# Performance work log

Measured on AMD Instinct MI355X. Metric: run time of the kernel, lower is better.

Reference implementation:

```python
import jax, jax.numpy as jnp
import numpy as np

H = 1024   # hidden_size
NH = 16    # num heads
HD = H // NH


def setup_inputs() -> dict:
    key = jax.random.key(0)
    ks = jax.random.split(key, 6)
    B, S = 4, 2048
    hidden_states = jax.random.normal(ks[0], (B, S, H), dtype=jnp.float32)
    attention_mask = jnp.zeros((B, S), dtype=jnp.float32)  # additive mask
    scale = 1.0 / np.sqrt(H)
    Wq = jax.random.normal(ks[1], (H, H), dtype=jnp.float32) * scale
    Wk = jax.random.normal(ks[2], (H, H), dtype=jnp.float32) * scale
    Wv = jax.random.normal(ks[3], (H, H), dtype=jnp.float32) * scale
    Wo = jax.random.normal(ks[4], (H, H), dtype=jnp.float32) * scale
    return {"hidden_states": hidden_states, "attention_mask": attention_mask,
            "Wq": Wq, "Wk": Wk, "Wv": Wv, "Wo": Wo}


def reference(hidden_states, attention_mask, Wq, Wk, Wv, Wo):
    B, S, _ = hidden_states.shape
    scaling = HD ** -0.5
    # nn.Linear: y = x @ W.T ; split heads -> [B, NH, S, HD]
    def heads(x, W):
        return (x @ W.T).reshape(B, S, NH, HD).transpose(0, 2, 1, 3)
    q = heads(hidden_states, Wq)
    k = heads(hidden_states, Wk)
    v = heads(hidden_states, Wv)
    scores = jnp.einsum('bhqd,bhkd->bhqk', q, k) * scaling
    scores = scores + attention_mask[:, None, None, :]
    weights = jax.nn.softmax(scores, axis=-1)
    attn = jnp.einsum('bhqk,bhkd->bhqd', weights, v)
    attn = attn.transpose(0, 2, 1, 3).reshape(B, S, H)
    return attn @ Wo.T
```

## Files before the change

### kernel.cpp

```cpp
#include <hip/hip_runtime.h>
#include <hip/hip_bf16.h>

#define B_ 4
#define S_ 2048
#define H_ 1024
#define NH_ 16
#define HD_ 64
#define QSCALE 0.1803368801111204f

typedef __bf16 bf16_t;
typedef bf16_t bf16x8 __attribute__((ext_vector_type(8)));
typedef bf16_t bf16x4 __attribute__((ext_vector_type(4)));
typedef float f32x4 __attribute__((ext_vector_type(4)));

__device__ __forceinline__ f32x4 mfma16(bf16x8 a, bf16x8 b, f32x4 c) {
  return __builtin_amdgcn_mfma_f32_16x16x32_bf16(a, b, c, 0, 0, 0);
}

__device__ __forceinline__ void gll16(const bf16_t* g, bf16_t* l) {
  __builtin_amdgcn_global_load_lds(
      (const __attribute__((address_space(1))) void*)g,
      (__attribute__((address_space(3))) void*)l, 16, 0, 0);
}

__device__ __forceinline__ bf16x8 frag64(const bf16_t* lds, int row,
                                         int kchunk) {
  return *(const bf16x8*)((const char*)lds + row * 128 +
                          ((kchunk ^ (row & 7)) << 4));
}

__device__ __forceinline__ void stage128(const bf16_t* gbase, int gstride,
                                         bf16_t* lds, int w, int lane) {
#pragma unroll
  for (int j = 0; j < 4; ++j) {
    int seg = w * 4 + j;
    int row = seg * 8 + (lane >> 3);
    int chunk = (lane & 7) ^ (row & 7);
    gll16(gbase + (size_t)row * gstride + chunk * 8, lds + seg * 512);
  }
}

__global__ __launch_bounds__(256) void cvt_all(
    const float* __restrict__ X, const float* __restrict__ Wq,
    const float* __restrict__ Wk, const float* __restrict__ Wv,
    const float* __restrict__ Wo,
    bf16_t* __restrict__ Xb, bf16_t* __restrict__ Wqb,
    bf16_t* __restrict__ Wkb, bf16_t* __restrict__ Wvb,
    bf16_t* __restrict__ Wob) {
  size_t i = ((size_t)blockIdx.x * 256 + threadIdx.x) * 4;
  const float* src;
  bf16_t* dst;
  size_t off;
  float scale = 1.0f;
  if (i < 8388608) {
    src = X; dst = Xb; off = i;
  } else {
    size_t j = i - 8388608;
    int w = (int)(j >> 20);
    off = j & 1048575;
    switch (w) {
      case 0: src = Wq; dst = Wqb; scale = QSCALE; break;
      case 1: src = Wk; dst = Wkb; break;
      case 2: src = Wv; dst = Wvb; break;
      default: src = Wo; dst = Wob; break;
    }
  }
  float4 v = *(const float4*)(src + off);
  bf16x4 o = {(bf16_t)(v.x * scale), (bf16_t)(v.y * scale),
              (bf16_t)(v.z * scale), (bf16_t)(v.w * scale)};
  *(bf16x4*)(dst + off) = o;
}

__device__ __forceinline__ void gemm_core(const bf16_t* __restrict__ A,
                                          const bf16_t* __restrict__ Bw,
                                          int Mb, int Nb, bf16_t* As,
                                          bf16_t* Bs, f32x4 (*acc)[4], int w,
                                          int lane, int quad, int l15, int wm,
                                          int wn) {
  for (int kb = 0; kb < 16; ++kb) {
    stage128(A + (size_t)Mb * 1024 + kb * 64, 1024, As, w, lane);
    stage128(Bw + (size_t)Nb * 1024 + kb * 64, 1024, Bs, w, lane);
    __syncthreads();
#pragma unroll
    for (int kt = 0; kt < 2; ++kt) {
      bf16x8 af[4], bfr[4];
#pragma unroll
      for (int i = 0; i < 4; ++i) {
        af[i] = frag64(As, wm * 64 + i * 16 + l15, kt * 4 + quad);
        bfr[i] = frag64(Bs, wn * 64 + i * 16 + l15, kt * 4 + quad);
      }
#pragma unroll
      for (int mt = 0; mt < 4; ++mt)
#pragma unroll
        for (int nt = 0; nt < 4; ++nt)
          acc[mt][nt] = mfma16(af[mt], bfr[nt], acc[mt][nt]);
    }
    __syncthreads();
  }
}

__global__ __launch_bounds__(256) void gemm_qkv(
    const bf16_t* __restrict__ Xb, const bf16_t* __restrict__ Wqb,
    const bf16_t* __restrict__ Wkb, const bf16_t* __restrict__ Wvb,
    bf16_t* __restrict__ q_ws, bf16_t* __restrict__ k_ws,
    bf16_t* __restrict__ vt_ws) {
  __shared__ __align__(16) bf16_t As[8192];
  __shared__ __align__(16) bf16_t Bs[8192];
  int w = threadIdx.x >> 6, lane = threadIdx.x & 63;
  int quad = lane >> 4, l15 = lane & 15;
  int wm = w >> 1, wn = w & 1;
  int z = blockIdx.z;
  const bf16_t* A = (z == 2) ? Wvb : Xb;
  const bf16_t* Bw = (z == 0) ? Wqb : ((z == 1) ? Wkb : Xb);
  int Mb = (z == 2) ? blockIdx.y * 128 : blockIdx.x * 128;
  int Nb = (z == 2) ? blockIdx.x * 128 : blockIdx.y * 128;
  f32x4 acc[4][4] = {};
  gemm_core(A, Bw, Mb, Nb, As, Bs, acc, w, lane, quad, l15, wm, wn);
  if (z != 2) {
    bf16_t* O = (z == 0) ? q_ws : k_ws;
#pragma unroll
    for (int mt = 0; mt < 4; ++mt) {
      int m0t = Mb + wm * 64 + mt * 16;
#pragma unroll
      for (int nt = 0; nt < 4; ++nt) {
        int n0t = Nb + wn * 64 + nt * 16;
        int h = n0t >> 6, d = (n0t & 63) + l15;
#pragma unroll
        for (int r = 0; r < 4; ++r) {
          int tok = m0t + quad * 4 + r;
          int b = tok >> 11, s = tok & 2047;
          O[(((size_t)b * NH_ + h) * S_ + s) * HD_ + d] = (bf16_t)acc[mt][nt][r];
        }
      }
    }
  } else {
#pragma unroll
    for (int mt = 0; mt < 4; ++mt) {
      int m0t = Mb + wm * 64 + mt * 16;
#pragma unroll
      for (int nt = 0; nt < 4; ++nt) {
        int n0t = Nb + wn * 64 + nt * 16;
#pragma unroll
        for (int r = 0; r < 4; ++r) {
          int dg = m0t + quad * 4 + r;
          int hh = dg >> 6, d = dg & 63;
          int tok = n0t + l15;
          int b = tok >> 11, s = tok & 2047;
          vt_ws[((size_t)(b * NH_ + hh) * HD_ + d) * S_ + s] =
              (bf16_t)acc[mt][nt][r];
        }
      }
    }
  }
}

__global__ __launch_bounds__(256) void gemm_out(
    const bf16_t* __restrict__ A, const bf16_t* __restrict__ Bw,
    float* __restrict__ out) {
  __shared__ __align__(16) bf16_t As[8192];
  __shared__ __align__(16) bf16_t Bs[8192];
  int w = threadIdx.x >> 6, lane = threadIdx.x & 63;
  int quad = lane >> 4, l15 = lane & 15;
  int wm = w >> 1, wn = w & 1;
  int Mb = blockIdx.x * 128, Nb = blockIdx.y * 128;
  f32x4 acc[4][4] = {};
  gemm_core(A, Bw, Mb, Nb, As, Bs, acc, w, lane, quad, l15, wm, wn);
#pragma unroll
  for (int mt = 0; mt < 4; ++mt) {
    int m0t = Mb + wm * 64 + mt * 16;
#pragma unroll
    for (int nt = 0; nt < 4; ++nt) {
      int n0t = Nb + wn * 64 + nt * 16;
#pragma unroll
      for (int r = 0; r < 4; ++r)
        out[(size_t)(m0t + quad * 4 + r) * 1024 + n0t + l15] = acc[mt][nt][r];
    }
  }
}

__global__ __launch_bounds__(256, 4) void attn_fused(
    const bf16_t* __restrict__ Q, const bf16_t* __restrict__ K,
    const bf16_t* __restrict__ Vt, const float* __restrict__ mask,
    bf16_t* __restrict__ Oa) {
  __shared__ __align__(16) bf16_t Ks[4096];
  __shared__ __align__(16) bf16_t Vs[4096];
  __shared__ __align__(16) bf16_t Ps[4][32 * 72];
  int w = threadIdx.x >> 6, lane = threadIdx.x & 63;
  int quad = lane >> 4, l15 = lane & 15;
  int bh = blockIdx.y;
  int b = bh >> 4, h = bh & 15;
  int q0 = blockIdx.x * 128 + w * 32;
  const bf16_t* Qh = Q + (size_t)bh * (S_ * HD_);
  const bf16_t* Kh = K + (size_t)bh * (S_ * HD_);
  const bf16_t* Vh = Vt + (size_t)bh * (HD_ * S_);
  const float* mb = mask + b * S_;
  bf16_t* pw = Ps[w];
  const float LOG2E = 1.4426950408889634f;
  const bf16_t one_b = (bf16_t)1.0f;
  bf16x8 ones = {one_b, one_b, one_b, one_b, one_b, one_b, one_b, one_b};

  int srow[2], schunk[2], soff[2];
#pragma unroll
  for (int j = 0; j < 2; ++j) {
    int seg = w * 2 + j;
    srow[j] = seg * 8 + (lane >> 3);
    schunk[j] = (lane & 7) ^ (srow[j] & 7);
    soff[j] = seg * 512 + lane * 8;
  }

  bf16x8 qf[2][2];
#pragma unroll
  for (int nt = 0; nt < 2; ++nt)
#pragma unroll
    for (int kt = 0; kt < 2; ++kt)
      qf[nt][kt] = *(const bf16x8*)(Qh + (size_t)(q0 + nt * 16 + l15) * HD_ +
                                    kt * 32 + quad * 8);

  f32x4 oc[4][2] = {};
  f32x4 lc[2] = {};

  bf16x8 kreg[2], vreg[2];
#pragma unroll
  for (int j = 0; j < 2; ++j) {
    kreg[j] = *(const bf16x8*)(Kh + (size_t)srow[j] * HD_ + schunk[j] * 8);
    vreg[j] = *(const bf16x8*)(Vh + (size_t)srow[j] * S_ + schunk[j] * 8);
  }

  for (int c = 0; c < 32; ++c) {
    __syncthreads();
#pragma unroll
    for (int j = 0; j < 2; ++j) {
      *(bf16x8*)(Ks + soff[j]) = kreg[j];
      *(bf16x8*)(Vs + soff[j]) = vreg[j];
    }
    __syncthreads();
    if (c + 1 < 32) {
      const bf16_t* Kc = Kh + (size_t)(c + 1) * 64 * HD_;
      const bf16_t* Vc = Vh + (size_t)(c + 1) * 64;
#pragma unroll
      for (int j = 0; j < 2; ++j) {
        kreg[j] = *(const bf16x8*)(Kc + (size_t)srow[j] * HD_ + schunk[j] * 8);
        vreg[j] = *(const bf16x8*)(Vc + (size_t)srow[j] * S_ + schunk[j] * 8);
      }
    }
    f32x4 sc[4][2] = {};
#pragma unroll
    for (int kt = 0; kt < 2; ++kt) {
      bf16x8 kf[4];
#pragma unroll
      for (int mt = 0; mt < 4; ++mt)
        kf[mt] = frag64(Ks, mt * 16 + l15, kt * 4 + quad);
#pragma unroll
      for (int mt = 0; mt < 4; ++mt)
#pragma unroll
        for (int nt = 0; nt < 2; ++nt)
          sc[mt][nt] = mfma16(kf[mt], qf[nt][kt], sc[mt][nt]);
    }
#pragma unroll
    for (int mt = 0; mt < 4; ++mt) {
      f32x4 mk = *(const f32x4*)(mb + c * 64 + mt * 16 + quad * 4);
      f32x4 mlv = mk * LOG2E;
#pragma unroll
      for (int nt = 0; nt < 2; ++nt) {
        f32x4 e = sc[mt][nt] + mlv;
        f32x4 p;
#pragma unroll
        for (int r = 0; r < 4; ++r) p[r] = __builtin_exp2f(e[r]);
        bf16x4 p4 = {(bf16_t)p[0], (bf16_t)p[1], (bf16_t)p[2], (bf16_t)p[3]};
        *(bf16x4*)(pw + (nt * 16 + l15) * 72 + mt * 16 + quad * 4) = p4;
      }
    }
#pragma unroll
    for (int kt = 0; kt < 2; ++kt) {
      bf16x8 pf[2];
#pragma unroll
      for (int nt = 0; nt < 2; ++nt)
        pf[nt] = *(const bf16x8*)(pw + (nt * 16 + l15) * 72 + kt * 32 +
                                  quad * 8);
      lc[0] = mfma16(ones, pf[0], lc[0]);
      lc[1] = mfma16(ones, pf[1], lc[1]);
#pragma unroll
      for (int dt = 0; dt < 4; ++dt) {
        bf16x8 vf = frag64(Vs, dt * 16 + l15, kt * 4 + quad);
#pragma unroll
        for (int nt = 0; nt < 2; ++nt)
          oc[dt][nt] = mfma16(vf, pf[nt], oc[dt][nt]);
      }
    }
  }
  float inv[2] = {1.0f / lc[0][0], 1.0f / lc[1][0]};
#pragma unroll
  for (int dt = 0; dt < 4; ++dt)
#pragma unroll
    for (int nt = 0; nt < 2; ++nt) {
      bf16x4 o4;
#pragma unroll
      for (int r = 0; r < 4; ++r) o4[r] = (bf16_t)(oc[dt][nt][r] * inv[nt]);
      size_t tok = (size_t)b * S_ + q0 + nt * 16 + l15;
      *(bf16x4*)(Oa + tok * H_ + h * HD_ + dt * 16 + quad * 4) = o4;
    }
}

extern "C" void kernel_launch(void* const* d_in, const int* in_sizes, int n_in,
                              void* d_out, int out_size, void* d_ws,
                              size_t ws_size, hipStream_t stream) {
  const float* hs   = (const float*)d_in[0];
  const float* mask = (const float*)d_in[1];
  const float* Wq   = (const float*)d_in[2];
  const float* Wk   = (const float*)d_in[3];
  const float* Wv   = (const float*)d_in[4];
  const float* Wo   = (const float*)d_in[5];
  float* out = (float*)d_out;

  char* p = (char*)d_ws;
  bf16_t* Xb  = (bf16_t*)p; p += (size_t)8192 * 1024 * 2;
  bf16_t* Wqb = (bf16_t*)p; p += (size_t)1024 * 1024 * 2;
  bf16_t* Wkb = (bf16_t*)p; p += (size_t)1024 * 1024 * 2;
  bf16_t* Wvb = (bf16_t*)p; p += (size_t)1024 * 1024 * 2;
  bf16_t* Wob = (bf16_t*)p; p += (size_t)1024 * 1024 * 2;
  bf16_t* q_ws  = (bf16_t*)p; p += (size_t)8192 * 1024 * 2;
  bf16_t* k_ws  = (bf16_t*)p; p += (size_t)8192 * 1024 * 2;
  bf16_t* vt_ws = (bf16_t*)p; p += (size_t)8192 * 1024 * 2;
  bf16_t* attn_b = Xb;

  cvt_all<<<12288, 256, 0, stream>>>(hs, Wq, Wk, Wv, Wo, Xb, Wqb, Wkb, Wvb,
                                     Wob);
  gemm_qkv<<<dim3(64, 8, 3), 256, 0, stream>>>(Xb, Wqb, Wkb, Wvb, q_ws, k_ws,
                                               vt_ws);
  attn_fused<<<dim3(16, 64), 256, 0, stream>>>(q_ws, k_ws, vt_ws, mask,
                                               attn_b);
  gemm_out<<<dim3(64, 8), 256, 0, stream>>>(attn_b, Wob, out);
}
```

Baseline: 298.9 us.

## Double-buffer K/V shared tiles and prefetch mask in attention kernel

Uses two LDS buffers for K and V so the next chunk is stored into the alternate buffer while the current one is consumed. This cuts the per-iteration barriers from two to one and prefetches global loads two chunks ahead. The mask values are also loaded one chunk early into registers. The cost is more LDS and registers, so launch bounds drop from 4 to 3 blocks per CU, which lowers occupancy.

Measured after the change: 292.2 us. 1.02x faster.

```diff
diff --git a/kernel.cpp b/kernel.cpp
--- a/kernel.cpp
+++ b/kernel.cpp
@@ -178,12 +178,12 @@
   }
 }
 
-__global__ __launch_bounds__(256, 4) void attn_fused(
+__global__ __launch_bounds__(256, 3) void attn_fused(
     const bf16_t* __restrict__ Q, const bf16_t* __restrict__ K,
     const bf16_t* __restrict__ Vt, const float* __restrict__ mask,
     bf16_t* __restrict__ Oa) {
-  __shared__ __align__(16) bf16_t Ks[4096];
-  __shared__ __align__(16) bf16_t Vs[4096];
+  __shared__ __align__(16) bf16_t Ks[2][4096];
+  __shared__ __align__(16) bf16_t Vs[2][4096];
   __shared__ __align__(16) bf16_t Ps[4][32 * 72];
   int w = threadIdx.x >> 6, lane = threadIdx.x & 63;
   int quad = lane >> 4, l15 = lane & 15;
@@ -225,31 +225,56 @@
     kreg[j] = *(const bf16x8*)(Kh + (size_t)srow[j] * HD_ + schunk[j] * 8);
     vreg[j] = *(const bf16x8*)(Vh + (size_t)srow[j] * S_ + schunk[j] * 8);
   }
+#pragma unroll
+  for (int j = 0; j < 2; ++j) {
+    *(bf16x8*)(&Ks[0][0] + soff[j]) = kreg[j];
+    *(bf16x8*)(&Vs[0][0] + soff[j]) = vreg[j];
+  }
+#pragma unroll
+  for (int j = 0; j < 2; ++j) {
+    kreg[j] = *(const bf16x8*)(Kh + (size_t)(64 * HD_) +
+                               (size_t)srow[j] * HD_ + schunk[j] * 8);
+    vreg[j] = *(const bf16x8*)(Vh + 64 + (size_t)srow[j] * S_ + schunk[j] * 8);
+  }
+  f32x4 mreg[4];
+#pragma unroll
+  for (int mt = 0; mt < 4; ++mt)
+    mreg[mt] = *(const f32x4*)(mb + mt * 16 + quad * 4);
+  __syncthreads();
 
   for (int c = 0; c < 32; ++c) {
-    __syncthreads();
-#pragma unroll
-    for (int j = 0; j < 2; ++j) {
-      *(bf16x8*)(Ks + soff[j]) = kreg[j];
-      *(bf16x8*)(Vs + soff[j]) = vreg[j];
-    }
-    __syncthreads();
+    int cur = c & 1;
     if (c + 1 < 32) {
-      const bf16_t* Kc = Kh + (size_t)(c + 1) * 64 * HD_;
-      const bf16_t* Vc = Vh + (size_t)(c + 1) * 64;
+#pragma unroll
+      for (int j = 0; j < 2; ++j) {
+        *(bf16x8*)(&Ks[cur ^ 1][0] + soff[j]) = kreg[j];
+        *(bf16x8*)(&Vs[cur ^ 1][0] + soff[j]) = vreg[j];
+      }
+    }
+    if (c + 2 < 32) {
+      const bf16_t* Kc = Kh + (size_t)(c + 2) * 64 * HD_;
+      const bf16_t* Vc = Vh + (size_t)(c + 2) * 64;
 #pragma unroll
       for (int j = 0; j < 2; ++j) {
         kreg[j] = *(const bf16x8*)(Kc + (size_t)srow[j] * HD_ + schunk[j] * 8);
         vreg[j] = *(const bf16x8*)(Vc + (size_t)srow[j] * S_ + schunk[j] * 8);
       }
     }
+    f32x4 mcur[4];
+#pragma unroll
+    for (int mt = 0; mt < 4; ++mt) mcur[mt] = mreg[mt];
+    if (c + 1 < 32) {
+#pragma unroll
+      for (int mt = 0; mt < 4; ++mt)
+        mreg[mt] = *(const f32x4*)(mb + (c + 1) * 64 + mt * 16 + quad * 4);
+    }
     f32x4 sc[4][2] = {};
 #pragma unroll
     for (int kt = 0; kt < 2; ++kt) {
       bf16x8 kf[4];
 #pragma unroll
       for (int mt = 0; mt < 4; ++mt)
-        kf[mt] = frag64(Ks, mt * 16 + l15, kt * 4 + quad);
+        kf[mt] = frag64(Ks[cur], mt * 16 + l15, kt * 4 + quad);
 #pragma unroll
       for (int mt = 0; mt < 4; ++mt)
 #pragma unroll
@@ -258,8 +283,7 @@
     }
 #pragma unroll
     for (int mt = 0; mt < 4; ++mt) {
-      f32x4 mk = *(const f32x4*)(mb + c * 64 + mt * 16 + quad * 4);
-      f32x4 mlv = mk * LOG2E;
+      f32x4 mlv = mcur[mt] * LOG2E;
 #pragma unroll
       for (int nt = 0; nt < 2; ++nt) {
         f32x4 e = sc[mt][nt] + mlv;
@@ -281,12 +305,13 @@
       lc[1] = mfma16(ones, pf[1], lc[1]);
 #pragma unroll
       for (int dt = 0; dt < 4; ++dt) {
-        bf16x8 vf = frag64(Vs, dt * 16 + l15, kt * 4 + quad);
+        bf16x8 vf = frag64(Vs[cur], dt * 16 + l15, kt * 4 + quad);
 #pragma unroll
         for (int nt = 0; nt < 2; ++nt)
           oc[dt][nt] = mfma16(vf, pf[nt], oc[dt][nt]);
       }
     }
+    __syncthreads();
   }
   float inv[2] = {1.0f / lc[0][0], 1.0f / lc[1][0]};
 #pragma unroll
```
